# Optimization experiments

Hardware: AMD Instinct MI355X
Metric: run time of the kernel (lower is better)

Reference implementation:

```python
import jax, jax.numpy as jnp
import numpy as np

N_EMBD = 2048
N_HEAD = 16
D_HEAD = N_EMBD // N_HEAD


def setup_inputs() -> dict:
    key = jax.random.key(0)
    k1, k2, k3 = jax.random.split(key, 3)
    x = jax.random.normal(k1, (2, 2048, N_EMBD), dtype=jnp.float32)
    # torch Linear stores weight as [out, in]; kept in that layout
    w_qkv = jax.random.normal(k2, (3 * N_EMBD, N_EMBD), dtype=jnp.float32) * (1.0 / np.sqrt(N_EMBD))
    w_out = jax.random.normal(k3, (N_EMBD, N_EMBD), dtype=jnp.float32) * (1.0 / np.sqrt(N_EMBD))
    return {"x": x, "w_qkv": w_qkv, "w_out": w_out}


def reference(x, w_qkv, w_out):
    B, T, C = x.shape
    H, D = N_HEAD, D_HEAD
    qkv = jnp.einsum('btc,oc->bto', x, w_qkv)            # [B,T,3C]
    qkv = qkv.reshape(B, T, 3, H, D)
    q = jnp.transpose(qkv[:, :, 0], (0, 2, 1, 3))        # [B,H,T,D]
    k = jnp.transpose(qkv[:, :, 1], (0, 2, 1, 3))
    v = jnp.transpose(qkv[:, :, 2], (0, 2, 1, 3))
    scale = 1.0 / np.sqrt(D).astype(np.float32)
    att = jnp.einsum('bhqd,bhkd->bhqk', q, k) * scale    # [B,H,T,T]
    causal = jnp.tril(jnp.ones((T, T), dtype=bool))
    att = jnp.where(causal[None, None], att, jnp.finfo(att.dtype).min)
    att = jax.nn.softmax(att, axis=-1)
    y = jnp.einsum('bhqk,bhkd->bhqd', att, v)            # [B,H,T,D]
    y = jnp.transpose(y, (0, 2, 1, 3)).reshape(B, T, C)
    return jnp.einsum('btc,oc->bto', y, w_out)
```

## Files before the change

### kernel.cpp

```cpp
#include <hip/hip_runtime.h>
#include <stdint.h>


typedef __attribute__((ext_vector_type(8))) short bf16x8;
typedef __attribute__((ext_vector_type(8))) unsigned short u16x8;
typedef __attribute__((ext_vector_type(4))) unsigned short u16x4;
typedef __attribute__((ext_vector_type(4))) float f32x4;

#define MFMA16(a, b, c) __builtin_amdgcn_mfma_f32_16x16x32_bf16((a), (b), (c), 0, 0, 0)

__device__ __forceinline__ unsigned short f2bf(float f) {
  union { float f; uint32_t u; } v; v.f = f;
  uint32_t r = v.u + 0x7FFFu + ((v.u >> 16) & 1u);
  return (unsigned short)(r >> 16);
}

__device__ __forceinline__ void gld_lds16(const unsigned short* g, unsigned short* lds) {
  __builtin_amdgcn_global_load_lds(
      (const __attribute__((address_space(1))) void*)g,
      (__attribute__((address_space(3))) void*)lds, 16, 0, 0);
}

__device__ __forceinline__ void cvt8(const float* __restrict__ in,
                                     unsigned short* __restrict__ out, int i) {
  float4 a = reinterpret_cast<const float4*>(in)[i * 2];
  float4 b = reinterpret_cast<const float4*>(in)[i * 2 + 1];
  u16x8 o;
  o[0] = f2bf(a.x); o[1] = f2bf(a.y); o[2] = f2bf(a.z); o[3] = f2bf(a.w);
  o[4] = f2bf(b.x); o[5] = f2bf(b.y); o[6] = f2bf(b.z); o[7] = f2bf(b.w);
  reinterpret_cast<u16x8*>(out)[i] = o;
}

__global__ __launch_bounds__(256) void cvt_all(const float* __restrict__ x,
                                               const float* __restrict__ wq,
                                               const float* __restrict__ wo,
                                               unsigned short* __restrict__ xb,
                                               unsigned short* __restrict__ wqb,
                                               unsigned short* __restrict__ wob) {
  const int stride = gridDim.x * blockDim.x;
  const int t0 = blockIdx.x * blockDim.x + threadIdx.x;
  for (int i = t0; i < 1048576; i += stride) cvt8(x, xb, i);
  for (int i = t0; i < 1572864; i += stride) cvt8(wq, wqb, i);
  for (int i = t0; i < 524288; i += stride) cvt8(wo, wob, i);
}

__device__ __forceinline__ void gemm128_core(const unsigned short* __restrict__ A,
                                             const unsigned short* __restrict__ Bt,
                                             int K, int brow, int bcol,
                                             unsigned short* lds_a, unsigned short* lds_b,
                                             f32x4 acc[4][4]) {
  const int tid = threadIdx.x;
  const int l   = tid & 63;
  const int w   = tid >> 6;
  const int wr  = (w >> 1) << 6;
  const int wc  = (w & 1) << 6;

  const int srow = tid >> 2;
  const int sswz = (tid & 3) ^ ((srow >> 1) & 3);
  const unsigned short* gA0 = A  + (size_t)(brow + srow) * K + 8 * sswz;
  const unsigned short* gA1 = gA0 + (size_t)64 * K;
  const unsigned short* gB0 = Bt + (size_t)(bcol + srow) * K + 8 * sswz;
  const unsigned short* gB1 = gB0 + (size_t)64 * K;

  unsigned short* la0 = lds_a + tid * 8;
  unsigned short* la1 = lds_a + (256 + tid) * 8;
  unsigned short* lb0 = lds_b + tid * 8;
  unsigned short* lb1 = lds_b + (256 + tid) * 8;

  const int fm    = l & 15;
  const int fswz8 = 8 * ((l >> 4) ^ ((fm >> 1) & 3));

  for (int k0 = 0; k0 < K; k0 += 32) {
    gld_lds16(gA0, la0);
    gld_lds16(gA1, la1);
    gld_lds16(gB0, lb0);
    gld_lds16(gB1, lb1);
    gA0 += 32; gA1 += 32; gB0 += 32; gB1 += 32;
    __syncthreads();
    bf16x8 af[4], bfv[4];
#pragma unroll
    for (int i = 0; i < 4; i++)
      af[i] = *(const bf16x8*)&lds_a[(wr + i * 16 + fm) * 32 + fswz8];
#pragma unroll
    for (int j = 0; j < 4; j++)
      bfv[j] = *(const bf16x8*)&lds_b[(wc + j * 16 + fm) * 32 + fswz8];
#pragma unroll
    for (int i = 0; i < 4; i++)
#pragma unroll
      for (int j = 0; j < 4; j++)
        acc[i][j] = MFMA16(af[i], bfv[j], acc[i][j]);
    __syncthreads();
  }
}

__global__ __launch_bounds__(256) void gemm_qkv(const unsigned short* __restrict__ xb,
                                                const unsigned short* __restrict__ wqb,
                                                unsigned short* __restrict__ Qb,
                                                unsigned short* __restrict__ Kb,
                                                unsigned short* __restrict__ Vtb) {
  __shared__ alignas(16) unsigned short lds_a[128 * 32];
  __shared__ alignas(16) unsigned short lds_b[128 * 32];
  f32x4 acc[4][4];
#pragma unroll
  for (int i = 0; i < 4; i++)
#pragma unroll
    for (int j = 0; j < 4; j++) acc[i][j] = (f32x4){0.f, 0.f, 0.f, 0.f};

  const int brow = blockIdx.y << 7;
  const int bcol = blockIdx.x << 7;
  gemm128_core(xb, wqb, 2048, brow, bcol, lds_a, lds_b, acc);

  const int l = threadIdx.x & 63;
  const int w = threadIdx.x >> 6;
  const int wr = (w >> 1) << 6, wc = (w & 1) << 6;
  const int which = bcol >> 11;
  const int bh = ((brow >> 11) << 4) | ((bcol >> 7) & 15);
  const int tbase = (brow & 2047) + wr + ((l >> 4) << 2);

#pragma unroll
  for (int i = 0; i < 4; i++) {
    const int t0 = tbase + i * 16;
#pragma unroll
    for (int j = 0; j < 4; j++) {
      const int d = wc + j * 16 + (l & 15);
      if (which == 2) {
        u16x4 pk;
#pragma unroll
        for (int r = 0; r < 4; r++) pk[r] = f2bf(acc[i][j][r]);
        *reinterpret_cast<u16x4*>(&Vtb[((size_t)bh * 128 + d) * 2048 + t0]) = pk;
      } else {
        unsigned short* dst = (which == 0 ? Qb : Kb) + ((size_t)bh * 2048 + t0) * 128 + d;
#pragma unroll
        for (int r = 0; r < 4; r++) dst[(size_t)r * 128] = f2bf(acc[i][j][r]);
      }
    }
  }
}

__global__ __launch_bounds__(256) void gemm_out(const unsigned short* __restrict__ yb,
                                                const unsigned short* __restrict__ wob,
                                                float* __restrict__ out) {
  __shared__ alignas(16) unsigned short lds_a[128 * 32];
  __shared__ alignas(16) unsigned short lds_b[128 * 32];
  f32x4 acc[4][4];
#pragma unroll
  for (int i = 0; i < 4; i++)
#pragma unroll
    for (int j = 0; j < 4; j++) acc[i][j] = (f32x4){0.f, 0.f, 0.f, 0.f};

  const int brow = blockIdx.y << 7;
  const int bcol = blockIdx.x << 7;
  gemm128_core(yb, wob, 2048, brow, bcol, lds_a, lds_b, acc);

  const int l = threadIdx.x & 63;
  const int w = threadIdx.x >> 6;
  const int wr = (w >> 1) << 6, wc = (w & 1) << 6;
#pragma unroll
  for (int i = 0; i < 4; i++) {
    const int m0 = brow + wr + i * 16 + ((l >> 4) << 2);
#pragma unroll
    for (int j = 0; j < 4; j++) {
      const int n = bcol + wc + j * 16 + (l & 15);
#pragma unroll
      for (int r = 0; r < 4; r++) out[(size_t)(m0 + r) * 2048 + n] = acc[i][j][r];
    }
  }
}

__device__ __forceinline__ void stage_kv64(const unsigned short* __restrict__ Kg,
                                           const unsigned short* __restrict__ Vg,
                                           int kv0, unsigned short* dk,
                                           unsigned short* dv, int tid) {
#pragma unroll
  for (int c = 0; c < 4; c++) {
    int s = c * 256 + tid;
    int row = s >> 4, g = s & 15;
    gld_lds16(&Kg[(size_t)(kv0 + row) * 128 + 8 * (g ^ (row & 7))], &dk[s * 8]);
  }
#pragma unroll
  for (int c = 0; c < 4; c++) {
    int s = c * 256 + tid;
    int row = s >> 3, g = s & 7;
    gld_lds16(&Vg[(size_t)row * 2048 + kv0 + 8 * (g ^ (row & 7))], &dv[s * 8]);
  }
}

__device__ __forceinline__ void attn_tile_step(const bf16x8 qf[4], f32x4 yacc[8],
                                               float mrow[4], float lsum[4],
                                               int qw0, int kv0,
                                               const unsigned short* kb,
                                               const unsigned short* vb,
                                               unsigned short* pw, int l) {
  const float SC = 0.12752585f;
  f32x4 sfr[4];
  __builtin_amdgcn_s_setprio(1);
#pragma unroll
  for (int kt = 0; kt < 4; kt++) {
    const int kr = kt * 16 + (l & 15);
    f32x4 s4 = (f32x4){0.f, 0.f, 0.f, 0.f};
#pragma unroll
    for (int ds = 0; ds < 4; ds++) {
      bf16x8 kfr = *(const bf16x8*)&kb[kr * 128 + 8 * (((ds << 2) + (l >> 4)) ^ (kr & 7))];
      s4 = MFMA16(qf[ds], kfr, s4);
    }
    sfr[kt] = s4;
  }
  __builtin_amdgcn_s_setprio(0);
  const bool need_mask = (kv0 + 63 > qw0);
#pragma unroll
  for (int kt = 0; kt < 4; kt++)
#pragma unroll
    for (int r = 0; r < 4; r++) {
      float sv = sfr[kt][r] * SC;
      if (need_mask) {
        int qa = qw0 + ((l >> 4) << 2) + r;
        int ka = kv0 + kt * 16 + (l & 15);
        sv = (ka > qa) ? -1e30f : sv;
      }
      sfr[kt][r] = sv;
    }
  float prmax[4];
#pragma unroll
  for (int r = 0; r < 4; r++)
    prmax[r] = fmaxf(fmaxf(sfr[0][r], sfr[1][r]), fmaxf(sfr[2][r], sfr[3][r]));
  bool sm = (prmax[0] <= mrow[0] + 8.f) && (prmax[1] <= mrow[1] + 8.f) &&
            (prmax[2] <= mrow[2] + 8.f) && (prmax[3] <= mrow[3] + 8.f);
  if (!__all(sm)) {
    float f[4];
#pragma unroll
    for (int r = 0; r < 4; r++) {
      float m = prmax[r];
      m = fmaxf(m, __shfl_xor(m, 1));
      m = fmaxf(m, __shfl_xor(m, 2));
      m = fmaxf(m, __shfl_xor(m, 4));
      m = fmaxf(m, __shfl_xor(m, 8));
      float mn = fmaxf(mrow[r], m);
      f[r] = exp2f(mrow[r] - mn);
      mrow[r] = mn;
      lsum[r] *= f[r];
    }
#pragma unroll
    for (int dt = 0; dt < 8; dt++)
#pragma unroll
      for (int r = 0; r < 4; r++) yacc[dt][r] *= f[r];
  }
#pragma unroll
  for (int kt = 0; kt < 4; kt++)
#pragma unroll
    for (int r = 0; r < 4; r++) {
      float p = exp2f(sfr[kt][r] - mrow[r]);
      lsum[r] += p;
      int row = ((l >> 4) << 2) + r;
      int k = kt * 16 + (l & 15);
      pw[row * 64 + (((k >> 3) ^ (row & 7)) << 3) + (k & 7)] = f2bf(p);
    }
  asm volatile("s_waitcnt lgkmcnt(0)" ::: "memory");
  __builtin_amdgcn_sched_barrier(0);
  __builtin_amdgcn_s_setprio(1);
#pragma unroll
  for (int ks = 0; ks < 2; ks++) {
    const int prow = l & 15;
    bf16x8 pa = *(const bf16x8*)&pw[prow * 64 + ((((ks << 2) + (l >> 4)) ^ (prow & 7)) << 3)];
#pragma unroll
    for (int dt = 0; dt < 8; dt++) {
      const int d = dt * 16 + (l & 15);
      bf16x8 vv = *(const bf16x8*)&vb[d * 64 + ((((ks << 2) + (l >> 4)) ^ (d & 7)) << 3)];
      yacc[dt] = MFMA16(pa, vv, yacc[dt]);
    }
  }
  __builtin_amdgcn_s_setprio(0);
}

__global__ __launch_bounds__(256, 2) void attn_kernel(const unsigned short* __restrict__ Qb,
                                                      const unsigned short* __restrict__ Kb,
                                                      const unsigned short* __restrict__ Vtb,
                                                      unsigned short* __restrict__ Yb) {
  __shared__ alignas(16) unsigned short lds_k[2][64 * 128];
  __shared__ alignas(16) unsigned short lds_v[2][128 * 64];
  __shared__ alignas(16) unsigned short p_lds[8][16 * 64];

  const int tid = threadIdx.x;
  const int l = tid & 63;
  const int w = tid >> 6;

  const int bid = blockIdx.x;
  const int xcd = bid & 7;
  const int loc = bid >> 3;
  const int bh = xcd * 4 + (loc >> 4);
  const int jidx = loc & 15;

  const int b = bh >> 4, h = bh & 15;

  const unsigned short* Qg = Qb + (size_t)bh * 2048 * 128;
  const unsigned short* Kg = Kb + (size_t)bh * 2048 * 128;
  const unsigned short* Vg = Vtb + (size_t)bh * 128 * 2048;

  const int j_lo = jidx, j_hi = 31 - jidx;
  const int qw0_lo = (j_lo << 6) + (w << 4);
  const int qw0_hi = (j_hi << 6) + (w << 4);

  bf16x8 qf_lo[4], qf_hi[4];
#pragma unroll
  for (int ds = 0; ds < 4; ds++) {
    qf_lo[ds] = *(const bf16x8*)&Qg[(size_t)(qw0_lo + (l & 15)) * 128 + ds * 32 + 8 * (l >> 4)];
    qf_hi[ds] = *(const bf16x8*)&Qg[(size_t)(qw0_hi + (l & 15)) * 128 + ds * 32 + 8 * (l >> 4)];
  }

  f32x4 yacc_lo[8], yacc_hi[8];
#pragma unroll
  for (int dt = 0; dt < 8; dt++) {
    yacc_lo[dt] = (f32x4){0.f, 0.f, 0.f, 0.f};
    yacc_hi[dt] = (f32x4){0.f, 0.f, 0.f, 0.f};
  }
  float mrow_lo[4], lsum_lo[4], mrow_hi[4], lsum_hi[4];
#pragma unroll
  for (int r = 0; r < 4; r++) {
    mrow_lo[r] = -1e30f; lsum_lo[r] = 0.f;
    mrow_hi[r] = -1e30f; lsum_hi[r] = 0.f;
  }

  const int nkv = j_hi + 1;

  stage_kv64(Kg, Vg, 0, lds_k[0], lds_v[0], tid);
  asm volatile("s_waitcnt vmcnt(0)" ::: "memory");
  __syncthreads();

  for (int t = 0; t < nkv; t++) {
    const int kv0 = t << 6;
    const int buf = t & 1;
    const unsigned short* kb = lds_k[buf];
    const unsigned short* vb = lds_v[buf];
    if (t + 1 < nkv)
      stage_kv64(Kg, Vg, kv0 + 64, lds_k[buf ^ 1], lds_v[buf ^ 1], tid);

    if (kv0 <= qw0_lo + 15)
      attn_tile_step(qf_lo, yacc_lo, mrow_lo, lsum_lo, qw0_lo, kv0, kb, vb, p_lds[w], l);
    attn_tile_step(qf_hi, yacc_hi, mrow_hi, lsum_hi, qw0_hi, kv0, kb, vb, p_lds[4 + w], l);

    asm volatile("s_waitcnt vmcnt(0)" ::: "memory");
    __syncthreads();
  }

  float lrow_lo[4], lrow_hi[4];
#pragma unroll
  for (int r = 0; r < 4; r++) {
    float s = lsum_lo[r];
    s += __shfl_xor(s, 1); s += __shfl_xor(s, 2);
    s += __shfl_xor(s, 4); s += __shfl_xor(s, 8);
    lrow_lo[r] = s;
    float u = lsum_hi[r];
    u += __shfl_xor(u, 1); u += __shfl_xor(u, 2);
    u += __shfl_xor(u, 4); u += __shfl_xor(u, 8);
    lrow_hi[r] = u;
  }
#pragma unroll
  for (int dt = 0; dt < 8; dt++)
#pragma unroll
    for (int r = 0; r < 4; r++) {
      int qa_lo = qw0_lo + ((l >> 4) << 2) + r;
      int qa_hi = qw0_hi + ((l >> 4) << 2) + r;
      Yb[((size_t)(b * 2048 + qa_lo)) * 2048 + h * 128 + dt * 16 + (l & 15)] =
          f2bf(yacc_lo[dt][r] / lrow_lo[r]);
      Yb[((size_t)(b * 2048 + qa_hi)) * 2048 + h * 128 + dt * 16 + (l & 15)] =
          f2bf(yacc_hi[dt][r] / lrow_hi[r]);
    }
}

extern "C" void kernel_launch(void* const* d_in, const int* in_sizes, int n_in,
                              void* d_out, int out_size, void* d_ws, size_t ws_size,
                              hipStream_t stream) {
  const float* x    = (const float*)d_in[0];
  const float* wqkv = (const float*)d_in[1];
  const float* wout = (const float*)d_in[2];
  float* out = (float*)d_out;

  unsigned short* ws  = (unsigned short*)d_ws;
  unsigned short* xb  = ws;
  unsigned short* wqb = xb + (size_t)8388608;
  unsigned short* wob = wqb + (size_t)12582912;
  unsigned short* Qb  = wob + (size_t)4194304;
  unsigned short* Kb  = Qb + (size_t)8388608;
  unsigned short* Vtb = Kb + (size_t)8388608;
  unsigned short* Yb  = Vtb + (size_t)8388608;

  cvt_all<<<2048, 256, 0, stream>>>(x, wqkv, wout, xb, wqb, wob);
  gemm_qkv<<<dim3(48, 32), 256, 0, stream>>>(xb, wqb, Qb, Kb, Vtb);
  attn_kernel<<<512, 256, 0, stream>>>(Qb, Kb, Vtb, Yb);
  gemm_out<<<dim3(16, 32), 256, 0, stream>>>(Yb, wob, out);
}
```

Baseline: 263.9 us.

## Split lo/hi query tiles across separate waves in 512-thread attention blocks

Each attention block now runs 8 waves instead of 4. Waves 0-3 handle the low (causally short) query tile and waves 4-7 handle the paired high tile, instead of each wave interleaving both tiles. This halves per-wave register state (one Q fragment, one accumulator set) so more waves can be resident, and K/V staging is split across 512 threads. The jidx mapping is also reversed for the second half of blocks per XCD to balance work. The risk is that the low-tile waves go idle once their causal range ends, while they still take part in every barrier. LDS per block is unchanged but occupancy may be limited by it.

```diff
diff --git a/kernel.cpp b/kernel.cpp
--- a/kernel.cpp
+++ b/kernel.cpp
@@ -172,14 +172,14 @@
                                            int kv0, unsigned short* dk,
                                            unsigned short* dv, int tid) {
 #pragma unroll
-  for (int c = 0; c < 4; c++) {
-    int s = c * 256 + tid;
+  for (int c = 0; c < 2; c++) {
+    int s = c * 512 + tid;
     int row = s >> 4, g = s & 15;
     gld_lds16(&Kg[(size_t)(kv0 + row) * 128 + 8 * (g ^ (row & 7))], &dk[s * 8]);
   }
 #pragma unroll
-  for (int c = 0; c < 4; c++) {
-    int s = c * 256 + tid;
+  for (int c = 0; c < 2; c++) {
+    int s = c * 512 + tid;
     int row = s >> 3, g = s & 7;
     gld_lds16(&Vg[(size_t)row * 2048 + kv0 + 8 * (g ^ (row & 7))], &dv[s * 8]);
   }
@@ -271,7 +271,7 @@
   __builtin_amdgcn_s_setprio(0);
 }
 
-__global__ __launch_bounds__(256, 2) void attn_kernel(const unsigned short* __restrict__ Qb,
+__global__ __launch_bounds__(512, 4) void attn_kernel(const unsigned short* __restrict__ Qb,
                                                       const unsigned short* __restrict__ Kb,
                                                       const unsigned short* __restrict__ Vtb,
                                                       unsigned short* __restrict__ Yb) {
@@ -287,7 +287,8 @@
   const int xcd = bid & 7;
   const int loc = bid >> 3;
   const int bh = xcd * 4 + (loc >> 4);
-  const int jidx = loc & 15;
+  const int jraw = loc & 15;
+  const int jidx = (loc < 32) ? jraw : (15 - jraw);
 
   const int b = bh >> 4, h = bh & 15;
 
@@ -295,31 +296,22 @@
   const unsigned short* Kg = Kb + (size_t)bh * 2048 * 128;
   const unsigned short* Vg = Vtb + (size_t)bh * 128 * 2048;
 
-  const int j_lo = jidx, j_hi = 31 - jidx;
-  const int qw0_lo = (j_lo << 6) + (w << 4);
-  const int qw0_hi = (j_hi << 6) + (w << 4);
-
-  bf16x8 qf_lo[4], qf_hi[4];
-#pragma unroll
-  for (int ds = 0; ds < 4; ds++) {
-    qf_lo[ds] = *(const bf16x8*)&Qg[(size_t)(qw0_lo + (l & 15)) * 128 + ds * 32 + 8 * (l >> 4)];
-    qf_hi[ds] = *(const bf16x8*)&Qg[(size_t)(qw0_hi + (l & 15)) * 128 + ds * 32 + 8 * (l >> 4)];
-  }
-
-  f32x4 yacc_lo[8], yacc_hi[8];
-#pragma unroll
-  for (int dt = 0; dt < 8; dt++) {
-    yacc_lo[dt] = (f32x4){0.f, 0.f, 0.f, 0.f};
-    yacc_hi[dt] = (f32x4){0.f, 0.f, 0.f, 0.f};
-  }
-  float mrow_lo[4], lsum_lo[4], mrow_hi[4], lsum_hi[4];
-#pragma unroll
-  for (int r = 0; r < 4; r++) {
-    mrow_lo[r] = -1e30f; lsum_lo[r] = 0.f;
-    mrow_hi[r] = -1e30f; lsum_hi[r] = 0.f;
-  }
-
-  const int nkv = j_hi + 1;
+  const int my_j = (w < 4) ? jidx : (31 - jidx);
+  const int qw0 = (my_j << 6) + ((w & 3) << 4);
+
+  bf16x8 qf[4];
+#pragma unroll
+  for (int ds = 0; ds < 4; ds++)
+    qf[ds] = *(const bf16x8*)&Qg[(size_t)(qw0 + (l & 15)) * 128 + ds * 32 + 8 * (l >> 4)];
+
+  f32x4 yacc[8];
+#pragma unroll
+  for (int dt = 0; dt < 8; dt++) yacc[dt] = (f32x4){0.f, 0.f, 0.f, 0.f};
+  float mrow[4], lsum[4];
+#pragma unroll
+  for (int r = 0; r < 4; r++) { mrow[r] = -1e30f; lsum[r] = 0.f; }
+
+  const int nkv = (31 - jidx) + 1;
 
   stage_kv64(Kg, Vg, 0, lds_k[0], lds_v[0], tid);
   asm volatile("s_waitcnt vmcnt(0)" ::: "memory");
@@ -328,41 +320,32 @@
   for (int t = 0; t < nkv; t++) {
     const int kv0 = t << 6;
     const int buf = t & 1;
-    const unsigned short* kb = lds_k[buf];
-    const unsigned short* vb = lds_v[buf];
     if (t + 1 < nkv)
       stage_kv64(Kg, Vg, kv0 + 64, lds_k[buf ^ 1], lds_v[buf ^ 1], tid);
 
-    if (kv0 <= qw0_lo + 15)
-      attn_tile_step(qf_lo, yacc_lo, mrow_lo, lsum_lo, qw0_lo, kv0, kb, vb, p_lds[w], l);
-    attn_tile_step(qf_hi, yacc_hi, mrow_hi, lsum_hi, qw0_hi, kv0, kb, vb, p_lds[4 + w], l);
+    if (kv0 <= qw0 + 15)
+      attn_tile_step(qf, yacc, mrow, lsum, qw0, kv0, lds_k[buf], lds_v[buf],
+                     p_lds[w], l);
 
     asm volatile("s_waitcnt vmcnt(0)" ::: "memory");
     __syncthreads();
   }
 
-  float lrow_lo[4], lrow_hi[4];
+  float lrow[4];
 #pragma unroll
   for (int r = 0; r < 4; r++) {
-    float s = lsum_lo[r];
+    float s = lsum[r];
     s += __shfl_xor(s, 1); s += __shfl_xor(s, 2);
     s += __shfl_xor(s, 4); s += __shfl_xor(s, 8);
-    lrow_lo[r] = s;
-    float u = lsum_hi[r];
-    u += __shfl_xor(u, 1); u += __shfl_xor(u, 2);
-    u += __shfl_xor(u, 4); u += __shfl_xor(u, 8);
-    lrow_hi[r] = u;
+    lrow[r] = s;
   }
 #pragma unroll
   for (int dt = 0; dt < 8; dt++)
 #pragma unroll
     for (int r = 0; r < 4; r++) {
-      int qa_lo = qw0_lo + ((l >> 4) << 2) + r;
-      int qa_hi = qw0_hi + ((l >> 4) << 2) + r;
-      Yb[((size_t)(b * 2048 + qa_lo)) * 2048 + h * 128 + dt * 16 + (l & 15)] =
-          f2bf(yacc_lo[dt][r] / lrow_lo[r]);
-      Yb[((size_t)(b * 2048 + qa_hi)) * 2048 + h * 128 + dt * 16 + (l & 15)] =
-          f2bf(yacc_hi[dt][r] / lrow_hi[r]);
+      int qa = qw0 + ((l >> 4) << 2) + r;
+      Yb[((size_t)(b * 2048 + qa)) * 2048 + h * 128 + dt * 16 + (l & 15)] =
+          f2bf(yacc[dt][r] / lrow[r]);
     }
 }
 
@@ -385,6 +368,6 @@
 
   cvt_all<<<2048, 256, 0, stream>>>(x, wqkv, wout, xb, wqb, wob);
   gemm_qkv<<<dim3(48, 32), 256, 0, stream>>>(xb, wqb, Qb, Kb, Vtb);
-  attn_kernel<<<512, 256, 0, stream>>>(Qb, Kb, Vtb, Yb);
+  attn_kernel<<<512, 512, 0, stream>>>(Qb, Kb, Vtb, Yb);
   gemm_out<<<dim3(16, 32), 256, 0, stream>>>(Yb, wob, out);
 }
```

Measured after the change: 262.3 us. Within noise of the previous version (-0.6%).
